# Kernel tuning notes

Measured on AMD Instinct MI355X. Metric: run time of the kernel, lower is better.

The kernel has to match this reference:

```python
import jax, jax.numpy as jnp
import numpy as np

NUM_CHANNEL_TYPES = 32  # global channel vocabulary (matches fill_max of channel_idx)


def setup_inputs() -> dict:
    key = jax.random.key(0)
    k1, k2, k3, k4, k5, k6 = jax.random.split(key, 6)
    B, C, H, W, E, P = 32, 8, 224, 224, 768, 16
    return {
        "x": jax.random.normal(k1, (B, C, H, W), dtype=jnp.float32),
        "channel_idx": jax.random.randint(k2, (B, C), 0, NUM_CHANNEL_TYPES, dtype=jnp.int64),
        "proj_w": jax.random.normal(k3, (E, P, P), dtype=jnp.float32) * 0.02,
        "proj_b": jax.random.normal(k4, (E,), dtype=jnp.float32) * 0.02,
        "ctx_w": jax.random.normal(k5, (E, E), dtype=jnp.float32) * 0.02,
        "ctx_b": jax.random.normal(k6, (E,), dtype=jnp.float32) * 0.02,
    }


def reference(x, channel_idx, proj_w, proj_b, ctx_w, ctx_b):
    B, C, H, W = x.shape
    E, P, _ = proj_w.shape
    Hp, Wp = H // P, W // P

    # Conv3d(1, E, kernel=(1,P,P), stride=(1,P,P)) == per-channel 2D patchify matmul
    xp = x.reshape(B, C, Hp, P, Wp, P)
    emb = jnp.einsum('bchpwq,epq->bechw', xp, proj_w) + proj_b[None, :, None, None, None]
    # emb: (B, E, C, Hp, Wp)

    # per-(sample, channel) average patch embedding -> (B, C, E)
    av_patch = emb.mean(axis=(3, 4)).transpose(0, 2, 1)
    flat = av_patch.reshape(B * C, E)
    seg = channel_idx.reshape(-1)

    # segment-mean over the batch by channel index (fused scatter-mean)
    sums = jax.ops.segment_sum(flat, seg, num_segments=NUM_CHANNEL_TYPES)
    cnt = jax.ops.segment_sum(jnp.ones((B * C,), flat.dtype), seg, num_segments=NUM_CHANNEL_TYPES)
    means = sums / jnp.maximum(cnt, 1.0)[:, None]
    chan_embed = means[seg].reshape(B, C, E)  # torch computes this under no_grad

    # context projection and broadcast-add back onto patch embeddings
    ctx = chan_embed @ ctx_w.T + ctx_b            # (B, C, E)
    out = emb + ctx.transpose(0, 2, 1)[:, :, :, None, None]

    # flatten(2).transpose(1, 2): (B, C*Hp*Wp, E)
    return out.reshape(B, E, C * Hp * Wp).transpose(0, 2, 1)
```

## Files before the change

kernel.cpp:

```cpp
#include <hip/hip_runtime.h>
#include <hip/hip_bf16.h>

typedef __attribute__((ext_vector_type(8))) short s16x8;
typedef __attribute__((ext_vector_type(4))) float f32x4;
typedef __attribute__((ext_vector_type(8))) unsigned short u16x8;
typedef __attribute__((ext_vector_type(4))) unsigned short u16x4;

static __device__ __forceinline__ unsigned short f2bf(float f) {
  unsigned int u = __float_as_uint(f);
  unsigned int r = u + 0x7fffu + ((u >> 16) & 1u);
  return (unsigned short)(r >> 16);
}
static __device__ __forceinline__ float bf2f(unsigned short s) {
  return __uint_as_float(((unsigned int)s) << 16);
}

static __device__ __forceinline__ void gload16(const void* g, void* l) {
  __builtin_amdgcn_global_load_lds(
      (const __attribute__((address_space(1))) unsigned int*)g,
      (__attribute__((address_space(3))) unsigned int*)l, 16, 0, 0);
}

__global__ __launch_bounds__(256) void k_mega(const float* __restrict__ x,
                                              unsigned short* __restrict__ xbf,
                                              float* __restrict__ avg3,
                                              const float* __restrict__ pw,
                                              unsigned short* __restrict__ pwbf,
                                              const float* __restrict__ cw,
                                              float* __restrict__ cwT) {
  __shared__ __align__(16) char smem[14 * 272 * 2];
  int b = blockIdx.x, t = threadIdx.x;
  if (b < 3584) {
    unsigned short* strip = (unsigned short*)smem;
    int bc = b / 14, hp = b - bc * 14;
    const float* img = x + ((size_t)bc * 224 + hp * 16) * 224;
    for (int idx = t; idx < 896; idx += 256) {
      int row = idx / 56, c4 = idx - row * 56;
      float4 v = reinterpret_cast<const float4*>(img + (size_t)row * 224)[c4];
      int wp = c4 >> 2, q0 = (c4 & 3) << 2;
      u16x4 pk = { f2bf(v.x), f2bf(v.y), f2bf(v.z), f2bf(v.w) };
      *(u16x4*)&strip[wp * 272 + row * 16 + q0] = pk;
    }
    __syncthreads();
    float acc = 0.f;
#pragma unroll
    for (int wp = 0; wp < 14; ++wp) acc += bf2f(strip[wp * 272 + t]);
    avg3[((size_t)bc * 14 + hp) * 256 + t] = acc;
    unsigned short* orow = xbf + ((size_t)bc * 196 + hp * 14) * 256;
    for (int i = t; i < 448; i += 256) {
      int patch = i >> 5, rem = i & 31;
      u16x8 v = *(const u16x8*)&strip[patch * 272 + (rem >> 1) * 16 + (rem & 1) * 8];
      *(u16x8*)(orow + i * 8) = v;
    }
  } else if (b < 3776) {
    int i = (b - 3584) * 256 + t;
    float4 v = reinterpret_cast<const float4*>(pw)[i];
    u16x4 pk = { f2bf(v.x), f2bf(v.y), f2bf(v.z), f2bf(v.w) };
    reinterpret_cast<u16x4*>(pwbf)[i] = pk;
  } else {
    float (*tile)[33] = (float(*)[33])smem;
    int bid2 = b - 3776;
    int bx = bid2 % 24, by = bid2 / 24;
    int tx = t & 31, ty = t >> 5;
#pragma unroll
    for (int k = 0; k < 4; ++k)
      tile[ty + 8 * k][tx] = cw[(size_t)(by * 32 + ty + 8 * k) * 768 + bx * 32 + tx];
    __syncthreads();
#pragma unroll
    for (int k = 0; k < 4; ++k)
      cwT[(size_t)(bx * 32 + ty + 8 * k) * 768 + by * 32 + tx] = tile[tx][ty + 8 * k];
  }
}

__global__ __launch_bounds__(256) void k_segmean(const float* __restrict__ avg3,
                                                 const int* __restrict__ seg,
                                                 float* __restrict__ sp) {
  __shared__ float red[4][64];
  __shared__ int rcnt[4];
  __shared__ int ssg[256];
  int s = blockIdx.x & 31, kc = blockIdx.x >> 5;
  int t = threadIdx.x;
  int kl = t & 63, slice = t >> 6;
  int k = kc * 64 + kl;
  ssg[t] = seg[t];
  __syncthreads();
  float sum = 0.f; int cnt = 0;
  for (int bc = slice * 64; bc < slice * 64 + 64; ++bc) {
    if (ssg[bc] == s) {
      ++cnt;
      const float* row = avg3 + (size_t)bc * 14 * 256 + k;
#pragma unroll
      for (int hp = 0; hp < 14; ++hp) sum += row[hp * 256];
    }
  }
  red[slice][kl] = sum;
  if (kl == 0) rcnt[slice] = cnt;
  __syncthreads();
  if (t < 64) {
    float tot = red[0][t] + red[1][t] + red[2][t] + red[3][t];
    int c = rcnt[0] + rcnt[1] + rcnt[2] + rcnt[3];
    sp[s * 256 + kc * 64 + t] = tot / (196.0f * (float)(c > 0 ? c : 1));
  }
}

__global__ __launch_bounds__(256) void k_means2(const float* __restrict__ sp,
                                                const float* __restrict__ pw,
                                                const float* __restrict__ pb,
                                                float* __restrict__ means) {
  __shared__ float ssp[256];
  __shared__ float red[8][32];
  int s = blockIdx.x & 31, e0 = (blockIdx.x >> 5) << 5;
  int t = threadIdx.x;
  int e = t & 31, ksl = t >> 5;
  ssp[t] = sp[s * 256 + t];
  __syncthreads();
  const float4* w = reinterpret_cast<const float4*>(pw + (size_t)(e0 + e) * 256 + ksl * 32);
  float a = 0.f;
#pragma unroll
  for (int j = 0; j < 8; ++j) {
    float4 v = w[j];
    int kb = ksl * 32 + j * 4;
    a += v.x * ssp[kb] + v.y * ssp[kb + 1] + v.z * ssp[kb + 2] + v.w * ssp[kb + 3];
  }
  red[ksl][e] = a;
  __syncthreads();
  if (t < 32) {
    float tot = 0.f;
#pragma unroll
    for (int j = 0; j < 8; ++j) tot += red[j][t];
    means[s * 768 + e0 + t] = tot + pb[e0 + t];
  }
}

__global__ __launch_bounds__(256) void k_ctx2(const float* __restrict__ means,
                                              const float* __restrict__ cwT,
                                              const float* __restrict__ cb,
                                              const float* __restrict__ pb,
                                              float* __restrict__ addv) {
  __shared__ float mn[768];
  __shared__ float red[8][32];
  int s = blockIdx.x & 31, e0 = (blockIdx.x >> 5) << 5;
  int t = threadIdx.x;
  int e = t & 31, fsl = t >> 5;
  mn[t] = means[s * 768 + t];
  mn[t + 256] = means[s * 768 + 256 + t];
  mn[t + 512] = means[s * 768 + 512 + t];
  __syncthreads();
  const float* col = cwT + (size_t)fsl * 96 * 768 + e0 + e;
  float a = 0.f;
#pragma unroll 8
  for (int j = 0; j < 96; ++j) a += mn[fsl * 96 + j] * col[(size_t)j * 768];
  red[fsl][e] = a;
  __syncthreads();
  if (t < 32) {
    float tot = 0.f;
#pragma unroll
    for (int j = 0; j < 8; ++j) tot += red[j][t];
    addv[s * 768 + e0 + t] = tot + cb[e0 + t] + pb[e0 + t];
  }
}

__global__ __launch_bounds__(256) void k_gemm(
    const unsigned short* __restrict__ xbf, const unsigned short* __restrict__ wbf,
    const float* __restrict__ addv, const int* __restrict__ seg,
    float* __restrict__ out) {
  __shared__ __align__(16) unsigned short Al[2][128 * 32];
  __shared__ __align__(16) unsigned short Bl[2][128 * 32];

  int bid = blockIdx.x;
  int xcd = bid & 7, local = bid >> 3;
  int mb = xcd * 49 + local / 6;
  int nb = local - (local / 6) * 6;
  int m0 = mb << 7, n0 = nb << 7;

  int t = threadIdx.x;
  int wave = t >> 6, lane = t & 63;
  int wm = (wave >> 1) << 6, wn = (wave & 1) << 6;
  int lr = lane & 15, hi = lane >> 4;

  int qswz = (lane & 3) ^ ((lane >> 2) & 3);
  const char* abase = (const char*)xbf + (size_t)(m0 + wave * 32 + (lane >> 2)) * 512 + qswz * 16;
  const char* bbase = (const char*)wbf + (size_t)(n0 + wave * 32 + (lane >> 2)) * 512 + qswz * 16;
  int ldso = wave * 2048;

  f32x4 acc[4][4] = {};

  gload16(abase, (char*)Al[0] + ldso);
  gload16(abase + 8192, (char*)Al[0] + ldso + 1024);
  gload16(bbase, (char*)Bl[0] + ldso);
  gload16(bbase + 8192, (char*)Bl[0] + ldso + 1024);
  __syncthreads();

#pragma unroll
  for (int kt = 0; kt < 8; ++kt) {
    int cur = kt & 1;
    if (kt < 7) {
      int nxt = cur ^ 1;
      const char* an = abase + (kt + 1) * 64;
      const char* bn = bbase + (kt + 1) * 64;
      gload16(an, (char*)Al[nxt] + ldso);
      gload16(an + 8192, (char*)Al[nxt] + ldso + 1024);
      gload16(bn, (char*)Bl[nxt] + ldso);
      gload16(bn + 8192, (char*)Bl[nxt] + ldso + 1024);
    }
    s16x8 af[4], bv[4];
    int qa = (hi ^ (lr & 3)) << 4;
#pragma unroll
    for (int i = 0; i < 4; ++i)
      af[i] = *(const s16x8*)((const char*)Al[cur] + (wm + i * 16 + lr) * 64 + qa);
#pragma unroll
    for (int j = 0; j < 4; ++j)
      bv[j] = *(const s16x8*)((const char*)Bl[cur] + (wn + j * 16 + lr) * 64 + qa);
#pragma unroll
    for (int i = 0; i < 4; ++i)
#pragma unroll
      for (int j = 0; j < 4; ++j)
        acc[i][j] = __builtin_amdgcn_mfma_f32_16x16x32_bf16(bv[j], af[i], acc[i][j], 0, 0, 0);
    __syncthreads();
  }

#pragma unroll
  for (int i = 0; i < 4; ++i) {
    int M = m0 + wm + i * 16 + lr;
    int sgi = seg[M / 196];
    const float* av = addv + (size_t)sgi * 768 + n0 + wn + hi * 4;
    float* orow = out + (size_t)M * 768 + n0 + wn + hi * 4;
#pragma unroll
    for (int j = 0; j < 4; ++j) {
      f32x4 a4 = *(const f32x4*)(av + j * 16);
      f32x4 v = acc[i][j];
      v.x += a4.x; v.y += a4.y; v.z += a4.z; v.w += a4.w;
      __builtin_nontemporal_store(v, (f32x4*)(orow + j * 16));
    }
  }
}

__global__ void k_cvt_fb(const float* __restrict__ in, unsigned short* __restrict__ o) {
  int i = blockIdx.x * 256 + threadIdx.x;
  float4 v = reinterpret_cast<const float4*>(in)[i];
  u16x4 pk = { f2bf(v.x), f2bf(v.y), f2bf(v.z), f2bf(v.w) };
  reinterpret_cast<u16x4*>(o)[i] = pk;
}

__global__ void k_transpose_fb(const float* __restrict__ in, float* __restrict__ out) {
  __shared__ float tile[32][33];
  int bx = blockIdx.x % 24, by = blockIdx.x / 24;
  int tx = threadIdx.x & 31, ty = threadIdx.x >> 5;
#pragma unroll
  for (int k = 0; k < 4; ++k)
    tile[ty + 8 * k][tx] = in[(size_t)(by * 32 + ty + 8 * k) * 768 + bx * 32 + tx];
  __syncthreads();
#pragma unroll
  for (int k = 0; k < 4; ++k)
    out[(size_t)(bx * 32 + ty + 8 * k) * 768 + by * 32 + tx] = tile[tx][ty + 8 * k];
}

__global__ void k_avgpatch_fb(const float* __restrict__ x, float* __restrict__ avg) {
  int bc = blockIdx.x;
  int k = threadIdx.x;
  int p = k >> 4, q = k & 15;
  const float* base = x + (size_t)bc * 224 * 224;
  float s = 0.f;
  for (int hp = 0; hp < 14; ++hp) {
    const float* row = base + (hp * 16 + p) * 224 + q;
#pragma unroll
    for (int wp = 0; wp < 14; ++wp) s += row[wp * 16];
  }
  avg[bc * 256 + k] = s * (1.0f / 196.0f);
}

__global__ __launch_bounds__(768) void k_chain_fb(const float* __restrict__ avg,
                                                  const int* __restrict__ seg,
                                                  const float* __restrict__ pw,
                                                  const float* __restrict__ pb,
                                                  const float* __restrict__ cwT,
                                                  const float* __restrict__ cb,
                                                  float* __restrict__ addv) {
  __shared__ float sp[256];
  __shared__ float mn[768];
  __shared__ int ssg[256];
  int s = blockIdx.x, t = threadIdx.x;
  if (t < 256) ssg[t] = seg[t];
  __syncthreads();
  if (t < 256) {
    float sum = 0.f; int c = 0;
    for (int bc = 0; bc < 256; ++bc)
      if (ssg[bc] == s) { sum += avg[bc * 256 + t]; ++c; }
    sp[t] = sum / (float)(c > 0 ? c : 1);
  }
  __syncthreads();
  {
    const float4* w = reinterpret_cast<const float4*>(pw + (size_t)t * 256);
    float a = 0.f;
#pragma unroll 8
    for (int k = 0; k < 64; ++k) {
      float4 v = w[k];
      a += v.x * sp[k * 4] + v.y * sp[k * 4 + 1] + v.z * sp[k * 4 + 2] + v.w * sp[k * 4 + 3];
    }
    mn[t] = a + pb[t];
  }
  __syncthreads();
  float a2 = 0.f;
#pragma unroll 8
  for (int f = 0; f < 768; ++f) a2 += mn[f] * cwT[(size_t)f * 768 + t];
  addv[s * 768 + t] = a2 + cb[t] + pb[t];
}

__global__ __launch_bounds__(256) void k_gemm_fb(
    const float* __restrict__ x, const unsigned short* __restrict__ wbf,
    const float* __restrict__ addv, const int* __restrict__ seg,
    float* __restrict__ out) {
  __shared__ unsigned short Al[128][40];
  __shared__ unsigned short Bl[128][40];
  int bid = blockIdx.x;
  int xcd = bid & 7, local = bid >> 3;
  int mb = xcd * 49 + local / 6;
  int nb = local - (local / 6) * 6;
  int m0 = mb << 7, n0 = nb << 7;
  int t = threadIdx.x;
  int wave = t >> 6, lane = t & 63;
  int wm = (wave >> 1) << 6, wn = (wave & 1) << 6;
  int lr = lane & 15, lk = (lane >> 4) << 3;
  int mstage = m0 + (t >> 1);
  int halfA = t & 1;
  int bc = mstage / 196;
  int pij = mstage - bc * 196;
  int hp = pij / 14;
  int wp = pij - hp * 14;
  const float* xbase = x + ((size_t)bc * 224 + hp * 16 + halfA) * 224 + wp * 16;
  const unsigned short* bsrc = wbf + (size_t)(n0 + (t >> 1)) * 256 + halfA * 16;
  unsigned short* adst = &Al[t >> 1][halfA * 16];
  unsigned short* bdst = &Bl[t >> 1][halfA * 16];
  f32x4 acc[4][4] = {};
  for (int ks = 0; ks < 8; ++ks) {
    __syncthreads();
    *(u16x8*)bdst       = *(const u16x8*)(bsrc + ks * 32);
    *(u16x8*)(bdst + 8) = *(const u16x8*)(bsrc + ks * 32 + 8);
    {
      const float4* src = reinterpret_cast<const float4*>(xbase + ks * 448);
      float4 v0 = src[0], v1 = src[1], v2 = src[2], v3 = src[3];
      u16x8 p0 = { f2bf(v0.x), f2bf(v0.y), f2bf(v0.z), f2bf(v0.w),
                   f2bf(v1.x), f2bf(v1.y), f2bf(v1.z), f2bf(v1.w) };
      u16x8 p1 = { f2bf(v2.x), f2bf(v2.y), f2bf(v2.z), f2bf(v2.w),
                   f2bf(v3.x), f2bf(v3.y), f2bf(v3.z), f2bf(v3.w) };
      *(u16x8*)adst = p0;
      *(u16x8*)(adst + 8) = p1;
    }
    __syncthreads();
    s16x8 af[4], bfv[4];
#pragma unroll
    for (int i = 0; i < 4; ++i) af[i] = *(const s16x8*)&Al[wm + i * 16 + lr][lk];
#pragma unroll
    for (int j = 0; j < 4; ++j) bfv[j] = *(const s16x8*)&Bl[wn + j * 16 + lr][lk];
#pragma unroll
    for (int i = 0; i < 4; ++i)
#pragma unroll
      for (int j = 0; j < 4; ++j)
        acc[i][j] = __builtin_amdgcn_mfma_f32_16x16x32_bf16(bfv[j], af[i], acc[i][j], 0, 0, 0);
  }
#pragma unroll
  for (int i = 0; i < 4; ++i) {
    int M = m0 + wm + i * 16 + lr;
    int sgi = seg[M / 196];
    int hi = lane >> 4;
    const float* av = addv + (size_t)sgi * 768 + n0 + wn + hi * 4;
    float* orow = out + (size_t)M * 768 + n0 + wn + hi * 4;
#pragma unroll
    for (int j = 0; j < 4; ++j) {
      f32x4 a4 = *(const f32x4*)(av + j * 16);
      f32x4 v = acc[i][j];
      v.x += a4.x; v.y += a4.y; v.z += a4.z; v.w += a4.w;
      *(f32x4*)(orow + j * 16) = v;
    }
  }
}


extern "C" void kernel_launch(void* const* d_in, const int* in_sizes, int n_in,
                              void* d_out, int out_size, void* d_ws, size_t ws_size,
                              hipStream_t stream) {
  (void)in_sizes; (void)n_in; (void)out_size;
  const float* x  = (const float*)d_in[0];
  const int*   sg = (const int*)d_in[1];
  const float* pw = (const float*)d_in[2];
  const float* pb = (const float*)d_in[3];
  const float* cw = (const float*)d_in[4];
  const float* cb = (const float*)d_in[5];
  float* out = (float*)d_out;

  char* ws = (char*)d_ws;
  unsigned short* pwbf = (unsigned short*)ws;
  float* cwT   = (float*)(ws + 393216);
  float* addv  = (float*)(ws + 2752512);
  float* sp    = (float*)(ws + 2850816);
  float* means = (float*)(ws + 2883584);
  float* avg3  = (float*)(ws + 2981888);
  unsigned short* xbf = (unsigned short*)(ws + 6651904);
  const size_t NEED = 6651904u + 25690112u;

  if (ws_size >= NEED) {
    k_mega<<<4352, 256, 0, stream>>>(x, xbf, avg3, pw, pwbf, cw, cwT);
    k_segmean<<<128, 256, 0, stream>>>(avg3, sg, sp);
    k_means2<<<768, 256, 0, stream>>>(sp, pw, pb, means);
    k_ctx2<<<768, 256, 0, stream>>>(means, cwT, cb, pb, addv);
    k_gemm<<<2352, 256, 0, stream>>>(xbf, pwbf, addv, sg, out);
  } else {
    float* avgp = (float*)(ws + 2981888);
    k_cvt_fb<<<192, 256, 0, stream>>>(pw, pwbf);
    k_transpose_fb<<<576, 256, 0, stream>>>(cw, cwT);
    k_avgpatch_fb<<<256, 256, 0, stream>>>(x, avgp);
    k_chain_fb<<<32, 768, 0, stream>>>(avgp, sg, pw, pb, cwT, cb, addv);
    k_gemm_fb<<<2352, 256, 0, stream>>>(x, pwbf, addv, sg, out);
  }
}
```

Measured before the change: 101.1 us.

## Triple-buffer GEMM LDS tiles with vmcnt waits and single barrier per k-step

The patch-embedding GEMM moves from double to triple-buffered LDS staging. It prefetches two k-tiles ahead and uses explicit s_waitcnt vmcnt plus one s_barrier per iteration instead of a trailing __syncthreads. The LDS swizzle is changed to a new XOR pattern on the source and read addresses to reduce bank conflicts, and output stores become normal stores instead of nontemporal. This adds LDS usage, and the manual vmcnt accounting can race if the count of in-flight loads is wrong.

```diff
diff --git a/kernel.cpp b/kernel.cpp
--- a/kernel.cpp
+++ b/kernel.cpp
@@ -164,8 +164,8 @@
     const unsigned short* __restrict__ xbf, const unsigned short* __restrict__ wbf,
     const float* __restrict__ addv, const int* __restrict__ seg,
     float* __restrict__ out) {
-  __shared__ __align__(16) unsigned short Al[2][128 * 32];
-  __shared__ __align__(16) unsigned short Bl[2][128 * 32];
+  __shared__ __align__(16) unsigned short Al[3][128 * 32];
+  __shared__ __align__(16) unsigned short Bl[3][128 * 32];
 
   int bid = blockIdx.x;
   int xcd = bid & 7, local = bid >> 3;
@@ -178,46 +178,56 @@
   int wm = (wave >> 1) << 6, wn = (wave & 1) << 6;
   int lr = lane & 15, hi = lane >> 4;
 
-  int qswz = (lane & 3) ^ ((lane >> 2) & 3);
-  const char* abase = (const char*)xbf + (size_t)(m0 + wave * 32 + (lane >> 2)) * 512 + qswz * 16;
-  const char* bbase = (const char*)wbf + (size_t)(n0 + wave * 32 + (lane >> 2)) * 512 + qswz * 16;
-  int ldso = wave * 2048;
+  int srcq = ((lane & 3) ^ ((lane >> 3) & 3)) << 4;
+  const char* abase0 = (const char*)xbf + (size_t)(m0 + wave * 32 + (lane >> 2)) * 512 + srcq;
+  const char* bbase0 = (const char*)wbf + (size_t)(n0 + wave * 32 + (lane >> 2)) * 512 + srcq;
+  int ldso = wave * 2048 + (lane & 31) * 16 + ((lane >> 5) << 10);
+  (void)ldso;
+
+#define STAGE(kt_, buf_)                                                        \
+  do {                                                                          \
+    const char* an = abase0 + (kt_) * 64;                                       \
+    const char* bn = bbase0 + (kt_) * 64;                                       \
+    gload16(an,         (char*)Al[buf_] + wave * 2048 + (lane << 4));           \
+    gload16(an + 8192,  (char*)Al[buf_] + wave * 2048 + 1024 + (lane << 4));    \
+    gload16(bn,         (char*)Bl[buf_] + wave * 2048 + (lane << 4));           \
+    gload16(bn + 8192,  (char*)Bl[buf_] + wave * 2048 + 1024 + (lane << 4));    \
+  } while (0)
 
   f32x4 acc[4][4] = {};
 
-  gload16(abase, (char*)Al[0] + ldso);
-  gload16(abase + 8192, (char*)Al[0] + ldso + 1024);
-  gload16(bbase, (char*)Bl[0] + ldso);
-  gload16(bbase + 8192, (char*)Bl[0] + ldso + 1024);
-  __syncthreads();
+  STAGE(0, 0);
+  STAGE(1, 1);
+
+  int rq = (hi ^ ((lr >> 1) & 3)) << 4;
 
 #pragma unroll
   for (int kt = 0; kt < 8; ++kt) {
-    int cur = kt & 1;
     if (kt < 7) {
-      int nxt = cur ^ 1;
-      const char* an = abase + (kt + 1) * 64;
-      const char* bn = bbase + (kt + 1) * 64;
-      gload16(an, (char*)Al[nxt] + ldso);
-      gload16(an + 8192, (char*)Al[nxt] + ldso + 1024);
-      gload16(bn, (char*)Bl[nxt] + ldso);
-      gload16(bn + 8192, (char*)Bl[nxt] + ldso + 1024);
-    }
+      asm volatile("s_waitcnt vmcnt(4)" ::: "memory");
+    } else {
+      asm volatile("s_waitcnt vmcnt(0)" ::: "memory");
+    }
+    __builtin_amdgcn_s_barrier();
+    if (kt + 2 < 8) {
+      int nb3 = (kt + 2) % 3;
+      STAGE(kt + 2, nb3);
+    }
+    int cur = kt % 3;
     s16x8 af[4], bv[4];
-    int qa = (hi ^ (lr & 3)) << 4;
 #pragma unroll
     for (int i = 0; i < 4; ++i)
-      af[i] = *(const s16x8*)((const char*)Al[cur] + (wm + i * 16 + lr) * 64 + qa);
+      af[i] = *(const s16x8*)((const char*)Al[cur] + (wm + i * 16 + lr) * 64 + rq);
 #pragma unroll
     for (int j = 0; j < 4; ++j)
-      bv[j] = *(const s16x8*)((const char*)Bl[cur] + (wn + j * 16 + lr) * 64 + qa);
+      bv[j] = *(const s16x8*)((const char*)Bl[cur] + (wn + j * 16 + lr) * 64 + rq);
 #pragma unroll
     for (int i = 0; i < 4; ++i)
 #pragma unroll
       for (int j = 0; j < 4; ++j)
         acc[i][j] = __builtin_amdgcn_mfma_f32_16x16x32_bf16(bv[j], af[i], acc[i][j], 0, 0, 0);
-    __syncthreads();
-  }
+  }
+#undef STAGE
 
 #pragma unroll
   for (int i = 0; i < 4; ++i) {
@@ -230,7 +240,7 @@
       f32x4 a4 = *(const f32x4*)(av + j * 16);
       f32x4 v = acc[i][j];
       v.x += a4.x; v.y += a4.y; v.z += a4.z; v.w += a4.w;
-      __builtin_nontemporal_store(v, (f32x4*)(orow + j * 16));
+      *(f32x4*)(orow + j * 16) = v;
     }
   }
 }
```

After: 89.75 us. 1.13x faster.
